# Kernel tuning notes

Hardware: AMD Instinct MI355X
Metric: run time of the kernel (lower is better)

Reference implementation:

```python
import jax, jax.numpy as jnp
import numpy as np

B, C, H, W = 32, 256, 8, 8
N = H * W                      # n_objects = 64
D_G_IN = 2 * C + 2             # pair concat + 2-dim relative position = 514
HG = 512                       # g hidden / output dim
HF = 512                       # f hidden dim
D_OUT = 256                    # f output dim


def _relative_grid_feat():
    # feat[p, q, 0] = oh(p) - oh(q); feat[p, q, 1] = ow(p) - ow(q); zero-centered globally
    idx = jnp.arange(N)
    oh, ow = idx // W, idx % W
    r0 = (oh[:, None] - oh[None, :]).astype(jnp.float32)
    r1 = (ow[:, None] - ow[None, :]).astype(jnp.float32)
    rel = jnp.stack([r0, r1], axis=-1)  # [N, N, 2]
    return rel - rel.mean()


def setup_inputs() -> dict:
    key = jax.random.key(0)
    ks = jax.random.split(key, 11)
    s = 0.02
    return {
        "x": jax.random.normal(ks[0], (B, C, H, W), dtype=jnp.float32),
        "g_W0": jax.random.normal(ks[1], (D_G_IN, HG), dtype=jnp.float32) * s,
        "g_b0": jnp.zeros((HG,), dtype=jnp.float32),
        "g_W1": jax.random.normal(ks[2], (HG, HG), dtype=jnp.float32) * s,
        "g_b1": jnp.zeros((HG,), dtype=jnp.float32),
        "g_W2": jax.random.normal(ks[3], (HG, HG), dtype=jnp.float32) * s,
        "g_b2": jnp.zeros((HG,), dtype=jnp.float32),
        "f_W0": jax.random.normal(ks[4], (HG, HF), dtype=jnp.float32) * s,
        "f_b0": jnp.zeros((HF,), dtype=jnp.float32),
        "f_W1": jax.random.normal(ks[5], (HF, D_OUT), dtype=jnp.float32) * s,
        "f_b1": jnp.zeros((D_OUT,), dtype=jnp.float32),
    }


def reference(x, g_W0, g_b0, g_W1, g_b1, g_W2, g_b2, f_W0, f_b0, f_W1, f_b1):
    relu = jax.nn.relu
    x_flat = x.reshape(B, C, N)                     # [B, C, N]
    xT = jnp.transpose(x_flat, (0, 2, 1))           # [B, N, C]
    # pair index k = p*N + q: xi takes object q (inner), xj takes object p (outer)
    xi = jnp.broadcast_to(xT[:, None, :, :], (B, N, N, C))
    xj = jnp.broadcast_to(xT[:, :, None, :], (B, N, N, C))
    rel = jnp.broadcast_to(_relative_grid_feat()[None], (B, N, N, 2))
    pair = jnp.concatenate([xi, xj, rel], axis=-1)  # [B, N, N, 2C+2]
    # g MLP (nonlinear=True -> activation on output too)
    h = relu(jnp.einsum('bpqd,dh->bpqh', pair, g_W0) + g_b0)
    h = relu(jnp.einsum('bpqh,hk->bpqk', h, g_W1) + g_b1)
    relations = relu(jnp.einsum('bpqh,hk->bpqk', h, g_W2) + g_b2)  # [B, N, N, HG]
    embedding = relations.sum(axis=(1, 2))          # sum over all pairs -> [B, HG]
    # f MLP (linear output)
    hf = relu(embedding @ f_W0 + f_b0)
    out = hf @ f_W1 + f_b1                          # [B, D_OUT]
    return out
```

## Files before the change

kernel.cpp:

```cpp
#include <hip/hip_runtime.h>


typedef short short8 __attribute__((ext_vector_type(8)));
typedef float f32x16 __attribute__((ext_vector_type(16)));

__device__ __forceinline__ unsigned short f2bf(float f) {
    unsigned u = __builtin_bit_cast(unsigned, f);
    u = (u + 0x7FFFu + ((u >> 16) & 1u)) >> 16;
    return (unsigned short)u;
}

__device__ __forceinline__ unsigned cvt_pk(float a, float b) {
    unsigned r;
    asm("v_cvt_pk_bf16_f32 %0, %1, %2" : "=v"(r) : "v"(a), "v"(b));
    return r;
}

__global__ __launch_bounds__(512) void uv_kernel(
    const float* __restrict__ x, const float* __restrict__ W0,
    const float* __restrict__ b0, float* __restrict__ Up, float* __restrict__ Vp)
{
    __shared__ float xs[256 * 8];
    const int blk = blockIdx.x;
    const int b = blk >> 3, n0 = (blk & 7) * 8;
    const int tid = threadIdx.x;

    for (int i = tid; i < 2048; i += 512) {
        int c = i >> 3, r = i & 7;
        xs[i] = x[((size_t)b * 256 + c) * 64 + n0 + r];
    }
    __syncthreads();

    const int h = tid;
    float ua[8], va[8];
#pragma unroll
    for (int r = 0; r < 8; ++r) { ua[r] = 0.f; va[r] = 0.f; }

#pragma unroll 4
    for (int c = 0; c < 256; ++c) {
        float wa = W0[(size_t)c * 512 + h];
        float wb = W0[(size_t)(256 + c) * 512 + h];
#pragma unroll
        for (int r = 0; r < 8; ++r) {
            float xv = xs[c * 8 + r];
            ua[r] += xv * wa;
            va[r] += xv * wb;
        }
    }
    const float w2a = W0[(size_t)512 * 512 + h];
    const float w2b = W0[(size_t)513 * 512 + h];
    const float bb = b0[h];
#pragma unroll
    for (int r = 0; r < 8; ++r) {
        int n = n0 + r;
        float fh = (float)(n >> 3), fw = (float)(n & 7);
        Up[((size_t)b * 64 + n) * 512 + h] = ua[r] - fh * w2a - fw * w2b;
        Vp[((size_t)b * 64 + n) * 512 + h] = va[r] + fh * w2a + fw * w2b + bb;
    }
}

__global__ __launch_bounds__(256) void wswz_kernel(
    const float* __restrict__ W1, const float* __restrict__ W2,
    unsigned short* __restrict__ W1s, unsigned short* __restrict__ W2s,
    float* __restrict__ emb)
{
    int gid = blockIdx.x * 256 + threadIdx.x;
    if (gid < 16384) emb[gid] = 0.f;
    int m = gid >> 15;
    int idx = gid & 32767;
    int col = idx & 511;
    int kg = idx >> 9;
    const float* W = m ? W2 : W1;
    unsigned short* O = m ? W2s : W1s;
    short8 v;
#pragma unroll
    for (int j = 0; j < 8; ++j)
        v[j] = (short)f2bf(W[(size_t)(kg * 8 + j) * 512 + col]);
    *(short8*)(O + (size_t)idx * 8) = v;
}

__global__ __launch_bounds__(512, 2) void main_kernel(
    const float* __restrict__ Up, const float* __restrict__ Vp,
    const unsigned short* __restrict__ W1s, const unsigned short* __restrict__ W2s,
    const float* __restrict__ b1, const float* __restrict__ b2,
    float* __restrict__ emb)
{
    extern __shared__ __align__(16) unsigned char lds[];
    unsigned char* T0 = lds;
    unsigned char* T1 = lds + 65536;

    const int wg = ((blockIdx.x & 7) << 7) | (blockIdx.x >> 3);
    const int b = wg >> 5, pp = wg & 31;
    const int p0 = pp * 2, p1 = p0 + 1;

    const int tid = threadIdx.x;
    const int lane = tid & 63, wave = tid >> 6;
    const int l31 = lane & 31, lg = lane >> 5;
    const int swz = (l31 & 15) << 4;
    const int wcol = wave * 64;

    {
        const int cc = tid & 63;
        const int r0 = tid >> 6;
        float4 u0[8], u1[8];
#pragma unroll
        for (int it = 0; it < 8; ++it) {
            const float* ub = Up + ((size_t)(b * 64 + r0 + it * 8)) * 512 + cc * 8;
            u0[it] = *(const float4*)(ub);
            u1[it] = *(const float4*)(ub + 4);
        }
        const float* vA = Vp + ((size_t)(b * 64 + p0)) * 512 + cc * 8;
        const float* vB = Vp + ((size_t)(b * 64 + p1)) * 512 + cc * 8;
        float4 vA0 = *(const float4*)(vA), vA1 = *(const float4*)(vA + 4);
        float4 vB0 = *(const float4*)(vB), vB1 = *(const float4*)(vB + 4);
#pragma unroll
        for (int it = 0; it < 8; ++it) {
            int row = r0 + it * 8;
            int off = row * 1024 + ((cc * 16) ^ ((row & 15) << 4));
            uint4 w;
            w.x = cvt_pk(fmaxf(u0[it].x + vA0.x, 0.f), fmaxf(u0[it].y + vA0.y, 0.f));
            w.y = cvt_pk(fmaxf(u0[it].z + vA0.z, 0.f), fmaxf(u0[it].w + vA0.w, 0.f));
            w.z = cvt_pk(fmaxf(u1[it].x + vA1.x, 0.f), fmaxf(u1[it].y + vA1.y, 0.f));
            w.w = cvt_pk(fmaxf(u1[it].z + vA1.z, 0.f), fmaxf(u1[it].w + vA1.w, 0.f));
            *(uint4*)(&T0[off]) = w;
            w.x = cvt_pk(fmaxf(u0[it].x + vB0.x, 0.f), fmaxf(u0[it].y + vB0.y, 0.f));
            w.y = cvt_pk(fmaxf(u0[it].z + vB0.z, 0.f), fmaxf(u0[it].w + vB0.w, 0.f));
            w.z = cvt_pk(fmaxf(u1[it].x + vB1.x, 0.f), fmaxf(u1[it].y + vB1.y, 0.f));
            w.w = cvt_pk(fmaxf(u1[it].z + vB1.z, 0.f), fmaxf(u1[it].w + vB1.w, 0.f));
            *(uint4*)(&T1[off]) = w;
        }
    }
    __syncthreads();

    const int arow0 = l31 * 1024;
    const int arow1 = (l31 + 32) * 1024;

    f32x16 acc[2][2][2];
#pragma unroll
    for (int t = 0; t < 2; ++t)
#pragma unroll
        for (int i = 0; i < 2; ++i)
#pragma unroll
            for (int j = 0; j < 2; ++j) acc[t][i][j] = (f32x16)0.f;

    {
        const unsigned short* wb = W1s + ((size_t)(lg * 512 + wcol + l31)) * 8;
        short8 wc0[2], wc1[2];
        wc0[0] = *(const short8*)(wb);
        wc1[0] = *(const short8*)(wb + 256);
        wc0[1] = *(const short8*)(wb + 8192);
        wc1[1] = *(const short8*)(wb + 8192 + 256);
        __builtin_amdgcn_s_setprio(1);
#pragma unroll
        for (int ks = 0; ks < 32; ++ks) {
            const int par = ks & 1;
            short8 cw0 = wc0[par], cw1 = wc1[par];
            if (ks < 30) {
                const unsigned short* np = wb + (size_t)(ks + 2) * 8192;
                wc0[par] = *(const short8*)(np);
                wc1[par] = *(const short8*)(np + 256);
            }
            int achunk = (ks * 32 + lg * 16) ^ swz;
            short8 a00 = *(const short8*)(&T0[arow0 + achunk]);
            short8 a01 = *(const short8*)(&T0[arow1 + achunk]);
            short8 a10 = *(const short8*)(&T1[arow0 + achunk]);
            short8 a11 = *(const short8*)(&T1[arow1 + achunk]);
            acc[0][0][0] = __builtin_amdgcn_mfma_f32_32x32x16_bf16(cw0, a00, acc[0][0][0], 0, 0, 0);
            acc[0][1][0] = __builtin_amdgcn_mfma_f32_32x32x16_bf16(cw1, a00, acc[0][1][0], 0, 0, 0);
            acc[0][0][1] = __builtin_amdgcn_mfma_f32_32x32x16_bf16(cw0, a01, acc[0][0][1], 0, 0, 0);
            acc[0][1][1] = __builtin_amdgcn_mfma_f32_32x32x16_bf16(cw1, a01, acc[0][1][1], 0, 0, 0);
            acc[1][0][0] = __builtin_amdgcn_mfma_f32_32x32x16_bf16(cw0, a10, acc[1][0][0], 0, 0, 0);
            acc[1][1][0] = __builtin_amdgcn_mfma_f32_32x32x16_bf16(cw1, a10, acc[1][1][0], 0, 0, 0);
            acc[1][0][1] = __builtin_amdgcn_mfma_f32_32x32x16_bf16(cw0, a11, acc[1][0][1], 0, 0, 0);
            acc[1][1][1] = __builtin_amdgcn_mfma_f32_32x32x16_bf16(cw1, a11, acc[1][1][1], 0, 0, 0);
        }
        __builtin_amdgcn_s_setprio(0);
    }
    __syncthreads();

    {
#pragma unroll
        for (int hf = 0; hf < 2; ++hf) {
#pragma unroll
            for (int g = 0; g < 4; ++g) {
                int h = wcol + hf * 32 + g * 8 + 4 * lg;
                float4 bb = *(const float4*)(b1 + h);
#pragma unroll
                for (int t = 0; t < 2; ++t) {
#pragma unroll
                    for (int qf = 0; qf < 2; ++qf) {
                        int q = qf * 32 + l31;
                        float a0 = fmaxf(acc[t][hf][qf][g * 4 + 0] + bb.x, 0.f);
                        float a1 = fmaxf(acc[t][hf][qf][g * 4 + 1] + bb.y, 0.f);
                        float a2 = fmaxf(acc[t][hf][qf][g * 4 + 2] + bb.z, 0.f);
                        float a3 = fmaxf(acc[t][hf][qf][g * 4 + 3] + bb.w, 0.f);
                        uint2 pk;
                        pk.x = cvt_pk(a0, a1);
                        pk.y = cvt_pk(a2, a3);
                        int off = q * 1024 + ((h * 2) ^ ((q & 15) << 4));
                        unsigned char* Tt = t ? T1 : T0;
                        *(uint2*)(&Tt[off]) = pk;
                    }
                }
            }
        }
    }
    __syncthreads();

    f32x16 acc2[2][2][2];
#pragma unroll
    for (int t = 0; t < 2; ++t)
#pragma unroll
        for (int i = 0; i < 2; ++i)
#pragma unroll
            for (int j = 0; j < 2; ++j) acc2[t][i][j] = (f32x16)0.f;

    {
        const unsigned short* wb = W2s + ((size_t)(lg * 512 + wcol + l31)) * 8;
        short8 wc0[2], wc1[2];
        wc0[0] = *(const short8*)(wb);
        wc1[0] = *(const short8*)(wb + 256);
        wc0[1] = *(const short8*)(wb + 8192);
        wc1[1] = *(const short8*)(wb + 8192 + 256);
        __builtin_amdgcn_s_setprio(1);
#pragma unroll
        for (int ks = 0; ks < 32; ++ks) {
            const int par = ks & 1;
            short8 cw0 = wc0[par], cw1 = wc1[par];
            if (ks < 30) {
                const unsigned short* np = wb + (size_t)(ks + 2) * 8192;
                wc0[par] = *(const short8*)(np);
                wc1[par] = *(const short8*)(np + 256);
            }
            int achunk = (ks * 32 + lg * 16) ^ swz;
            short8 a00 = *(const short8*)(&T0[arow0 + achunk]);
            short8 a01 = *(const short8*)(&T0[arow1 + achunk]);
            short8 a10 = *(const short8*)(&T1[arow0 + achunk]);
            short8 a11 = *(const short8*)(&T1[arow1 + achunk]);
            acc2[0][0][0] = __builtin_amdgcn_mfma_f32_32x32x16_bf16(a00, cw0, acc2[0][0][0], 0, 0, 0);
            acc2[0][1][0] = __builtin_amdgcn_mfma_f32_32x32x16_bf16(a01, cw0, acc2[0][1][0], 0, 0, 0);
            acc2[0][0][1] = __builtin_amdgcn_mfma_f32_32x32x16_bf16(a00, cw1, acc2[0][0][1], 0, 0, 0);
            acc2[0][1][1] = __builtin_amdgcn_mfma_f32_32x32x16_bf16(a01, cw1, acc2[0][1][1], 0, 0, 0);
            acc2[1][0][0] = __builtin_amdgcn_mfma_f32_32x32x16_bf16(a10, cw0, acc2[1][0][0], 0, 0, 0);
            acc2[1][1][0] = __builtin_amdgcn_mfma_f32_32x32x16_bf16(a11, cw0, acc2[1][1][0], 0, 0, 0);
            acc2[1][0][1] = __builtin_amdgcn_mfma_f32_32x32x16_bf16(a10, cw1, acc2[1][0][1], 0, 0, 0);
            acc2[1][1][1] = __builtin_amdgcn_mfma_f32_32x32x16_bf16(a11, cw1, acc2[1][1][1], 0, 0, 0);
        }
        __builtin_amdgcn_s_setprio(0);
    }

    {
        float s[2];
#pragma unroll
        for (int cf = 0; cf < 2; ++cf) {
            int col = wcol + cf * 32 + l31;
            float bias = b2[col];
            float tt = 0.f;
#pragma unroll
            for (int t = 0; t < 2; ++t)
#pragma unroll
                for (int rf = 0; rf < 2; ++rf)
#pragma unroll
                    for (int reg = 0; reg < 16; ++reg)
                        tt += fmaxf(acc2[t][rf][cf][reg] + bias, 0.f);
            tt += __shfl_xor(tt, 32);
            s[cf] = tt;
        }
        if (lane < 32) {
            unsafeAtomicAdd(&emb[b * 512 + wcol + lane], s[0]);
            unsafeAtomicAdd(&emb[b * 512 + wcol + 32 + lane], s[1]);
        }
    }
}

__global__ __launch_bounds__(256) void f0_kernel(
    const float* __restrict__ emb, const float* __restrict__ fW0,
    const float* __restrict__ fb0, float* __restrict__ hs)
{
    __shared__ float es[512];
    __shared__ float red[256];
    const int b = blockIdx.x >> 3, s = blockIdx.x & 7;
    const int t = threadIdx.x;
    const int colL = t & 63, cg = t >> 6;
    es[t] = emb[b * 512 + t];
    es[t + 256] = emb[b * 512 + 256 + t];
    __syncthreads();
    const int col = s * 64 + colL;
    float a = 0.f;
    const int c0 = cg * 128;
#pragma unroll 4
    for (int c = c0; c < c0 + 128; ++c)
        a += es[c] * fW0[(size_t)c * 512 + col];
    red[t] = a;
    __syncthreads();
    if (t < 64) {
        float r = red[t] + red[t + 64] + red[t + 128] + red[t + 192] + fb0[col];
        hs[b * 512 + col] = fmaxf(r, 0.f);
    }
}

__global__ __launch_bounds__(256) void f1_kernel(
    const float* __restrict__ hs, const float* __restrict__ fW1,
    const float* __restrict__ fb1, float* __restrict__ out)
{
    __shared__ float es[512];
    __shared__ float red[256];
    const int b = blockIdx.x >> 2, s = blockIdx.x & 3;
    const int t = threadIdx.x;
    const int colL = t & 63, cg = t >> 6;
    es[t] = hs[b * 512 + t];
    es[t + 256] = hs[b * 512 + 256 + t];
    __syncthreads();
    const int col = s * 64 + colL;
    float a = 0.f;
    const int c0 = cg * 128;
#pragma unroll 4
    for (int c = c0; c < c0 + 128; ++c)
        a += es[c] * fW1[(size_t)c * 256 + col];
    red[t] = a;
    __syncthreads();
    if (t < 64) {
        out[b * 256 + col] = red[t] + red[t + 64] + red[t + 128] + red[t + 192] + fb1[col];
    }
}

extern "C" void kernel_launch(void* const* d_in, const int* in_sizes, int n_in,
                              void* d_out, int out_size, void* d_ws, size_t ws_size,
                              hipStream_t stream)
{
    const float* x   = (const float*)d_in[0];
    const float* gW0 = (const float*)d_in[1];
    const float* gb0 = (const float*)d_in[2];
    const float* gW1 = (const float*)d_in[3];
    const float* gb1 = (const float*)d_in[4];
    const float* gW2 = (const float*)d_in[5];
    const float* gb2 = (const float*)d_in[6];
    const float* fW0 = (const float*)d_in[7];
    const float* fb0 = (const float*)d_in[8];
    const float* fW1 = (const float*)d_in[9];
    const float* fb1 = (const float*)d_in[10];
    float* out = (float*)d_out;

    char* ws = (char*)d_ws;
    float* Up           = (float*)(ws);
    float* Vp           = (float*)(ws + (4 << 20));
    unsigned short* W1s = (unsigned short*)(ws + (8 << 20));
    unsigned short* W2s = (unsigned short*)(ws + (8 << 20) + (512 << 10));
    float* emb          = (float*)(ws + (9 << 20));
    float* hs           = (float*)(ws + (9 << 20) + (64 << 10));

    uv_kernel<<<256, 512, 0, stream>>>(x, gW0, gb0, Up, Vp);
    wswz_kernel<<<256, 256, 0, stream>>>(gW1, gW2, W1s, W2s, emb);
    main_kernel<<<1024, 512, 131072, stream>>>(Up, Vp, W1s, W2s, gb1, gb2, emb);
    f0_kernel<<<256, 256, 0, stream>>>(emb, fW0, fb0, hs);
    f1_kernel<<<128, 256, 0, stream>>>(hs, fW1, fb1, out);
}
```

Before: 172.1 us.

## Replicate swizzled weights per XCD and remap uv blocks to XCD-local batches

The weight-swizzle kernel now writes eight copies of the bf16 W1/W2 tiles, one per XCD, and the main kernel reads the copy matching its blockIdx&7. Each XCD's L2 then serves its own weight replica instead of all XCDs contending for one copy, and the uv kernel's batch mapping is remapped so each XCD produces the Up/Vp rows its main-kernel blocks consume. The cost is eight times more weight-conversion work and workspace, which adds time to the swizzle kernel.

```diff
diff --git a/kernel.cpp b/kernel.cpp
--- a/kernel.cpp
+++ b/kernel.cpp
@@ -21,8 +21,10 @@
     const float* __restrict__ b0, float* __restrict__ Up, float* __restrict__ Vp)
 {
     __shared__ float xs[256 * 8];
-    const int blk = blockIdx.x;
-    const int b = blk >> 3, n0 = (blk & 7) * 8;
+    const int xcd = blockIdx.x & 7;
+    const int j = blockIdx.x >> 3;
+    const int b = (xcd << 2) | (j >> 3);
+    const int n0 = (j & 7) * 8;
     const int tid = threadIdx.x;
 
     for (int i = tid; i < 2048; i += 512) {
@@ -61,17 +63,20 @@
 
 __global__ __launch_bounds__(256) void wswz_kernel(
     const float* __restrict__ W1, const float* __restrict__ W2,
-    unsigned short* __restrict__ W1s, unsigned short* __restrict__ W2s,
+    unsigned short* __restrict__ W1s8, unsigned short* __restrict__ W2s8,
     float* __restrict__ emb)
 {
+    const int rep = blockIdx.x & 7;
+    const int inner = (blockIdx.x >> 3) * 256 + threadIdx.x;
     int gid = blockIdx.x * 256 + threadIdx.x;
     if (gid < 16384) emb[gid] = 0.f;
-    int m = gid >> 15;
-    int idx = gid & 32767;
+
+    int m = inner >> 15;
+    int idx = inner & 32767;
     int col = idx & 511;
     int kg = idx >> 9;
     const float* W = m ? W2 : W1;
-    unsigned short* O = m ? W2s : W1s;
+    unsigned short* O = (m ? W2s8 : W1s8) + (size_t)rep * 262144;
     short8 v;
 #pragma unroll
     for (int j = 0; j < 8; ++j)
@@ -81,7 +86,7 @@
 
 __global__ __launch_bounds__(512, 2) void main_kernel(
     const float* __restrict__ Up, const float* __restrict__ Vp,
-    const unsigned short* __restrict__ W1s, const unsigned short* __restrict__ W2s,
+    const unsigned short* __restrict__ W1s8, const unsigned short* __restrict__ W2s8,
     const float* __restrict__ b1, const float* __restrict__ b2,
     float* __restrict__ emb)
 {
@@ -92,6 +97,9 @@
     const int wg = ((blockIdx.x & 7) << 7) | (blockIdx.x >> 3);
     const int b = wg >> 5, pp = wg & 31;
     const int p0 = pp * 2, p1 = p0 + 1;
+
+    const unsigned short* W1r = W1s8 + (size_t)(blockIdx.x & 7) * 262144;
+    const unsigned short* W2r = W2s8 + (size_t)(blockIdx.x & 7) * 262144;
 
     const int tid = threadIdx.x;
     const int lane = tid & 63, wave = tid >> 6;
@@ -144,7 +152,7 @@
             for (int j = 0; j < 2; ++j) acc[t][i][j] = (f32x16)0.f;
 
     {
-        const unsigned short* wb = W1s + ((size_t)(lg * 512 + wcol + l31)) * 8;
+        const unsigned short* wb = W1r + ((size_t)(lg * 512 + wcol + l31)) * 8;
         short8 wc0[2], wc1[2];
         wc0[0] = *(const short8*)(wb);
         wc1[0] = *(const short8*)(wb + 256);
@@ -216,7 +224,7 @@
             for (int j = 0; j < 2; ++j) acc2[t][i][j] = (f32x16)0.f;
 
     {
-        const unsigned short* wb = W2s + ((size_t)(lg * 512 + wcol + l31)) * 8;
+        const unsigned short* wb = W2r + ((size_t)(lg * 512 + wcol + l31)) * 8;
         short8 wc0[2], wc1[2];
         wc0[0] = *(const short8*)(wb);
         wc1[0] = *(const short8*)(wb + 256);
@@ -342,16 +350,16 @@
     float* out = (float*)d_out;
 
     char* ws = (char*)d_ws;
-    float* Up           = (float*)(ws);
-    float* Vp           = (float*)(ws + (4 << 20));
-    unsigned short* W1s = (unsigned short*)(ws + (8 << 20));
-    unsigned short* W2s = (unsigned short*)(ws + (8 << 20) + (512 << 10));
-    float* emb          = (float*)(ws + (9 << 20));
-    float* hs           = (float*)(ws + (9 << 20) + (64 << 10));
+    float* Up            = (float*)(ws);
+    float* Vp            = (float*)(ws + (4 << 20));
+    unsigned short* W1s8 = (unsigned short*)(ws + (8 << 20));
+    unsigned short* W2s8 = (unsigned short*)(ws + (12 << 20));
+    float* emb           = (float*)(ws + (16 << 20));
+    float* hs            = (float*)(ws + (16 << 20) + (64 << 10));
 
     uv_kernel<<<256, 512, 0, stream>>>(x, gW0, gb0, Up, Vp);
-    wswz_kernel<<<256, 256, 0, stream>>>(gW1, gW2, W1s, W2s, emb);
-    main_kernel<<<1024, 512, 131072, stream>>>(Up, Vp, W1s, W2s, gb1, gb2, emb);
+    wswz_kernel<<<2048, 256, 0, stream>>>(gW1, gW2, W1s8, W2s8, emb);
+    main_kernel<<<1024, 512, 131072, stream>>>(Up, Vp, W1s8, W2s8, gb1, gb2, emb);
     f0_kernel<<<256, 256, 0, stream>>>(emb, fW0, fb0, hs);
     f1_kernel<<<128, 256, 0, stream>>>(hs, fW1, fb1, out);
 }
```

Measured after the change: 174.0 us. Within noise of the previous version (+1.1%).

## Compute first-layer U/V projections with bf16 MFMA and fuse f MLP kernels

Applied to the files above, without the earlier changes.

The scalar fp32 uv_kernel is replaced by an MFMA bf16 GEMM (uv_gemm_kernel), one block per batch, which reads W0 pre-converted to bf16 in a swizzled layout. Converting W0 is folded into the existing W1/W2 conversion kernel. The two f-MLP kernels are merged into a single per-batch kernel, so one launch and the hs round trip go away. This cuts FP32 ALU time and launch overhead in the small kernels. In exchange the first-layer projections now run in bf16 precision, and the uv GEMM uses only 32 blocks.

```diff
diff --git a/kernel.cpp b/kernel.cpp
--- a/kernel.cpp
+++ b/kernel.cpp
@@ -16,55 +16,31 @@
     return r;
 }
 
-__global__ __launch_bounds__(512) void uv_kernel(
-    const float* __restrict__ x, const float* __restrict__ W0,
-    const float* __restrict__ b0, float* __restrict__ Up, float* __restrict__ Vp)
+__global__ __launch_bounds__(512) void wcvt_kernel(
+    const float* __restrict__ W0, const float* __restrict__ W1,
+    const float* __restrict__ W2,
+    unsigned short* __restrict__ W0s, unsigned short* __restrict__ W1s,
+    unsigned short* __restrict__ W2s, float* __restrict__ emb)
 {
-    __shared__ float xs[256 * 8];
-    const int blk = blockIdx.x;
-    const int b = blk >> 3, n0 = (blk & 7) * 8;
     const int tid = threadIdx.x;
-
-    for (int i = tid; i < 2048; i += 512) {
-        int c = i >> 3, r = i & 7;
-        xs[i] = x[((size_t)b * 256 + c) * 64 + n0 + r];
-    }
-    __syncthreads();
-
-    const int h = tid;
-    float ua[8], va[8];
-#pragma unroll
-    for (int r = 0; r < 8; ++r) { ua[r] = 0.f; va[r] = 0.f; }
-
-#pragma unroll 4
-    for (int c = 0; c < 256; ++c) {
-        float wa = W0[(size_t)c * 512 + h];
-        float wb = W0[(size_t)(256 + c) * 512 + h];
-#pragma unroll
-        for (int r = 0; r < 8; ++r) {
-            float xv = xs[c * 8 + r];
-            ua[r] += xv * wa;
-            va[r] += xv * wb;
-        }
-    }
-    const float w2a = W0[(size_t)512 * 512 + h];
-    const float w2b = W0[(size_t)513 * 512 + h];
-    const float bb = b0[h];
-#pragma unroll
-    for (int r = 0; r < 8; ++r) {
-        int n = n0 + r;
-        float fh = (float)(n >> 3), fw = (float)(n & 7);
-        Up[((size_t)b * 64 + n) * 512 + h] = ua[r] - fh * w2a - fw * w2b;
-        Vp[((size_t)b * 64 + n) * 512 + h] = va[r] + fh * w2a + fw * w2b + bb;
-    }
-}
-
-__global__ __launch_bounds__(256) void wswz_kernel(
-    const float* __restrict__ W1, const float* __restrict__ W2,
-    unsigned short* __restrict__ W1s, unsigned short* __restrict__ W2s,
-    float* __restrict__ emb)
-{
-    int gid = blockIdx.x * 256 + threadIdx.x;
+    if (blockIdx.x < 64) {
+        int gid = blockIdx.x * 512 + tid;
+        int kg = gid >> 10, hp = gid & 1023;
+        short8 v;
+        if (hp < 512) {
+#pragma unroll
+            for (int j = 0; j < 8; ++j)
+                v[j] = (short)f2bf(W0[(size_t)(kg * 8 + j) * 512 + hp]);
+        } else {
+            int h = hp - 512;
+#pragma unroll
+            for (int j = 0; j < 8; ++j)
+                v[j] = (short)f2bf(W0[(size_t)(256 + kg * 8 + j) * 512 + h]);
+        }
+        *(short8*)(W0s + (size_t)gid * 8) = v;
+        return;
+    }
+    int gid = (blockIdx.x - 64) * 512 + tid;
     if (gid < 16384) emb[gid] = 0.f;
     int m = gid >> 15;
     int idx = gid & 32767;
@@ -77,6 +53,118 @@
     for (int j = 0; j < 8; ++j)
         v[j] = (short)f2bf(W[(size_t)(kg * 8 + j) * 512 + col]);
     *(short8*)(O + (size_t)idx * 8) = v;
+}
+
+__global__ __launch_bounds__(512, 2) void uv_gemm_kernel(
+    const float* __restrict__ x, const unsigned short* __restrict__ W0s,
+    const float* __restrict__ W0, const float* __restrict__ b0,
+    float* __restrict__ Up, float* __restrict__ Vp)
+{
+    __shared__ __align__(16) unsigned char X[64 * 512];
+
+    const int b = blockIdx.x;
+    const int tid = threadIdx.x;
+    const int lane = tid & 63, wave = tid >> 6;
+    const int l31 = lane & 31, lg = lane >> 5;
+    const int swz = (l31 & 15) << 4;
+    const int wvcol = wave * 128;
+
+    {
+        const int n = tid & 63, cg = tid >> 6;
+        const float* xb = x + (size_t)b * 16384 + n;
+#pragma unroll
+        for (int ch = 0; ch < 4; ++ch) {
+            int c0 = cg * 32 + ch * 8;
+            float v0 = xb[(c0 + 0) * 64], v1 = xb[(c0 + 1) * 64];
+            float v2 = xb[(c0 + 2) * 64], v3 = xb[(c0 + 3) * 64];
+            float v4 = xb[(c0 + 4) * 64], v5 = xb[(c0 + 5) * 64];
+            float v6 = xb[(c0 + 6) * 64], v7 = xb[(c0 + 7) * 64];
+            uint4 w;
+            w.x = cvt_pk(v0, v1); w.y = cvt_pk(v2, v3);
+            w.z = cvt_pk(v4, v5); w.w = cvt_pk(v6, v7);
+            int cchunk = cg * 4 + ch;
+            int off = n * 512 + ((cchunk * 16) ^ ((n & 15) << 4));
+            *(uint4*)(&X[off]) = w;
+        }
+    }
+    __syncthreads();
+
+    const int arow0 = l31 * 512;
+    const int arow1 = (l31 + 32) * 512;
+
+    f32x16 acc[4][2];
+#pragma unroll
+    for (int i = 0; i < 4; ++i)
+#pragma unroll
+        for (int j = 0; j < 2; ++j) acc[i][j] = (f32x16)0.f;
+
+    {
+        const unsigned short* wb = W0s + ((size_t)(lg * 1024 + wvcol + l31)) * 8;
+        short8 wc0[2], wc1[2], wc2[2], wc3[2];
+        wc0[0] = *(const short8*)(wb);
+        wc1[0] = *(const short8*)(wb + 256);
+        wc2[0] = *(const short8*)(wb + 512);
+        wc3[0] = *(const short8*)(wb + 768);
+        wc0[1] = *(const short8*)(wb + 16384);
+        wc1[1] = *(const short8*)(wb + 16384 + 256);
+        wc2[1] = *(const short8*)(wb + 16384 + 512);
+        wc3[1] = *(const short8*)(wb + 16384 + 768);
+        __builtin_amdgcn_s_setprio(1);
+#pragma unroll
+        for (int ks = 0; ks < 16; ++ks) {
+            const int par = ks & 1;
+            short8 cw0 = wc0[par], cw1 = wc1[par], cw2 = wc2[par], cw3 = wc3[par];
+            if (ks < 14) {
+                const unsigned short* np = wb + (size_t)(ks + 2) * 16384;
+                wc0[par] = *(const short8*)(np);
+                wc1[par] = *(const short8*)(np + 256);
+                wc2[par] = *(const short8*)(np + 512);
+                wc3[par] = *(const short8*)(np + 768);
+            }
+            int achunk = (ks * 32 + lg * 16) ^ swz;
+            short8 a0 = *(const short8*)(&X[arow0 + achunk]);
+            short8 a1 = *(const short8*)(&X[arow1 + achunk]);
+            acc[0][0] = __builtin_amdgcn_mfma_f32_32x32x16_bf16(cw0, a0, acc[0][0], 0, 0, 0);
+            acc[1][0] = __builtin_amdgcn_mfma_f32_32x32x16_bf16(cw1, a0, acc[1][0], 0, 0, 0);
+            acc[2][0] = __builtin_amdgcn_mfma_f32_32x32x16_bf16(cw2, a0, acc[2][0], 0, 0, 0);
+            acc[3][0] = __builtin_amdgcn_mfma_f32_32x32x16_bf16(cw3, a0, acc[3][0], 0, 0, 0);
+            acc[0][1] = __builtin_amdgcn_mfma_f32_32x32x16_bf16(cw0, a1, acc[0][1], 0, 0, 0);
+            acc[1][1] = __builtin_amdgcn_mfma_f32_32x32x16_bf16(cw1, a1, acc[1][1], 0, 0, 0);
+            acc[2][1] = __builtin_amdgcn_mfma_f32_32x32x16_bf16(cw2, a1, acc[2][1], 0, 0, 0);
+            acc[3][1] = __builtin_amdgcn_mfma_f32_32x32x16_bf16(cw3, a1, acc[3][1], 0, 0, 0);
+        }
+        __builtin_amdgcn_s_setprio(0);
+    }
+
+    {
+        const bool isV = (wvcol >= 512);
+        float* dst = isV ? Vp : Up;
+        const float sgn = isV ? 1.f : -1.f;
+#pragma unroll
+        for (int hf = 0; hf < 4; ++hf) {
+#pragma unroll
+            for (int g = 0; g < 4; ++g) {
+                int hb = wvcol + hf * 32 + g * 8 + 4 * lg;
+                int hq = hb & 511;
+                float4 wa = *(const float4*)(W0 + (size_t)512 * 512 + hq);
+                float4 wb4 = *(const float4*)(W0 + (size_t)513 * 512 + hq);
+                float4 bb;
+                if (isV) bb = *(const float4*)(b0 + hq);
+                else { bb.x = 0.f; bb.y = 0.f; bb.z = 0.f; bb.w = 0.f; }
+#pragma unroll
+                for (int nf = 0; nf < 2; ++nf) {
+                    int n = nf * 32 + l31;
+                    float fh = (float)(n >> 3), fw = (float)(n & 7);
+                    float4 o;
+                    o.x = acc[hf][nf][g * 4 + 0] + sgn * (fh * wa.x + fw * wb4.x) + bb.x;
+                    o.y = acc[hf][nf][g * 4 + 1] + sgn * (fh * wa.y + fw * wb4.y) + bb.y;
+                    o.z = acc[hf][nf][g * 4 + 2] + sgn * (fh * wa.z + fw * wb4.z) + bb.z;
+                    o.w = acc[hf][nf][g * 4 + 3] + sgn * (fh * wa.w + fw * wb4.w) + bb.w;
+                    *(float4*)(&dst[((size_t)(b * 64 + n)) * 512 + hq]) = o;
+                }
+            }
+        }
+    }
 }
 
 __global__ __launch_bounds__(512, 2) void main_kernel(
@@ -273,55 +361,42 @@
     }
 }
 
-__global__ __launch_bounds__(256) void f0_kernel(
+__global__ __launch_bounds__(1024) void f_kernel(
     const float* __restrict__ emb, const float* __restrict__ fW0,
-    const float* __restrict__ fb0, float* __restrict__ hs)
-{
-    __shared__ float es[512];
-    __shared__ float red[256];
-    const int b = blockIdx.x >> 3, s = blockIdx.x & 7;
-    const int t = threadIdx.x;
-    const int colL = t & 63, cg = t >> 6;
-    es[t] = emb[b * 512 + t];
-    es[t + 256] = emb[b * 512 + 256 + t];
-    __syncthreads();
-    const int col = s * 64 + colL;
-    float a = 0.f;
-    const int c0 = cg * 128;
-#pragma unroll 4
-    for (int c = c0; c < c0 + 128; ++c)
-        a += es[c] * fW0[(size_t)c * 512 + col];
-    red[t] = a;
-    __syncthreads();
-    if (t < 64) {
-        float r = red[t] + red[t + 64] + red[t + 128] + red[t + 192] + fb0[col];
-        hs[b * 512 + col] = fmaxf(r, 0.f);
-    }
-}
-
-__global__ __launch_bounds__(256) void f1_kernel(
-    const float* __restrict__ hs, const float* __restrict__ fW1,
+    const float* __restrict__ fb0, const float* __restrict__ fW1,
     const float* __restrict__ fb1, float* __restrict__ out)
 {
     __shared__ float es[512];
-    __shared__ float red[256];
-    const int b = blockIdx.x >> 2, s = blockIdx.x & 3;
-    const int t = threadIdx.x;
-    const int colL = t & 63, cg = t >> 6;
-    es[t] = hs[b * 512 + t];
-    es[t + 256] = hs[b * 512 + 256 + t];
-    __syncthreads();
-    const int col = s * 64 + colL;
-    float a = 0.f;
-    const int c0 = cg * 128;
+    __shared__ float red[1024];
+    __shared__ float hs[512];
+    const int b = blockIdx.x, tid = threadIdx.x;
+
+    if (tid < 512) es[tid] = emb[b * 512 + tid];
+    __syncthreads();
+    {
+        int col = tid & 511, half = tid >> 9;
+        float a = half ? 0.f : fb0[col];
+        int c0 = half * 256;
 #pragma unroll 4
-    for (int c = c0; c < c0 + 128; ++c)
-        a += es[c] * fW1[(size_t)c * 256 + col];
-    red[t] = a;
-    __syncthreads();
-    if (t < 64) {
-        out[b * 256 + col] = red[t] + red[t + 64] + red[t + 128] + red[t + 192] + fb1[col];
-    }
+        for (int c = c0; c < c0 + 256; ++c)
+            a += es[c] * fW0[(size_t)c * 512 + col];
+        red[tid] = a;
+    }
+    __syncthreads();
+    if (tid < 512) hs[tid] = fmaxf(red[tid] + red[tid + 512], 0.f);
+    __syncthreads();
+    {
+        int col = tid & 255, q = tid >> 8;
+        float a = q ? 0.f : fb1[col];
+        int c0 = q * 128;
+#pragma unroll 4
+        for (int c = c0; c < c0 + 128; ++c)
+            a += hs[c] * fW1[(size_t)c * 256 + col];
+        red[tid] = a;
+    }
+    __syncthreads();
+    if (tid < 256)
+        out[b * 256 + tid] = red[tid] + red[tid + 256] + red[tid + 512] + red[tid + 768];
 }
 
 extern "C" void kernel_launch(void* const* d_in, const int* in_sizes, int n_in,
@@ -346,12 +421,11 @@
     float* Vp           = (float*)(ws + (4 << 20));
     unsigned short* W1s = (unsigned short*)(ws + (8 << 20));
     unsigned short* W2s = (unsigned short*)(ws + (8 << 20) + (512 << 10));
-    float* emb          = (float*)(ws + (9 << 20));
-    float* hs           = (float*)(ws + (9 << 20) + (64 << 10));
-
-    uv_kernel<<<256, 512, 0, stream>>>(x, gW0, gb0, Up, Vp);
-    wswz_kernel<<<256, 256, 0, stream>>>(gW1, gW2, W1s, W2s, emb);
+    unsigned short* W0s = (unsigned short*)(ws + (9 << 20));
+    float* emb          = (float*)(ws + (9 << 20) + (512 << 10));
+
+    wcvt_kernel<<<192, 512, 0, stream>>>(gW0, gW1, gW2, W0s, W1s, W2s, emb);
+    uv_gemm_kernel<<<32, 512, 0, stream>>>(x, W0s, gW0, gb0, Up, Vp);
     main_kernel<<<1024, 512, 131072, stream>>>(Up, Vp, W1s, W2s, gb1, gb2, emb);
-    f0_kernel<<<256, 256, 0, stream>>>(emb, fW0, fb0, hs);
-    f1_kernel<<<128, 256, 0, stream>>>(hs, fW1, fb1, out);
-}
+    f_kernel<<<32, 1024, 0, stream>>>(emb, fW0, fb0, fW1, fb1, out);
+}
```

Result: no change. 174.4 us (+1.3%).
